# Kernel optimization log

Measured on AMD Instinct MI355X. Metric: run time of the kernel, lower is better.

The kernel has to match this reference:

```python
import jax, jax.numpy as jnp
import numpy as np

N, E, D = 50000, 800000, 128
H, C = 8, 16  # heads, hidden_per_head; H*C == D
NEG_SLOPE = 0.15


def setup_inputs() -> dict:
    key = jax.random.key(0)
    ks = jax.random.split(key, 8)
    x = jax.random.normal(ks[0], (N, D), dtype=jnp.float32)
    edge_index = jax.random.randint(ks[1], (2, E), 0, N, dtype=jnp.int32)
    s = 1.0 / np.sqrt(D)
    return {
        "x": x,
        "edge_index": edge_index,
        "ln_g": jnp.ones((D,), jnp.float32),
        "ln_b": jnp.zeros((D,), jnp.float32),
        "W_l": jax.random.normal(ks[2], (D, H * C), jnp.float32) * s,
        "b_l": jnp.zeros((H * C,), jnp.float32),
        "W_r": jax.random.normal(ks[3], (D, H * C), jnp.float32) * s,
        "b_r": jnp.zeros((H * C,), jnp.float32),
        "att": jax.random.normal(ks[4], (H, C), jnp.float32) * (1.0 / np.sqrt(C)),
        "bias": jnp.zeros((H * C,), jnp.float32),
    }


def _layernorm(x, g, b, eps=1e-5):
    mu = jnp.mean(x, axis=-1, keepdims=True)
    var = jnp.mean(jnp.square(x - mu), axis=-1, keepdims=True)
    return (x - mu) * jax.lax.rsqrt(var + eps) * g + b


def reference(x, edge_index, ln_g, ln_b, W_l, b_l, W_r, b_r, att, bias):
    src, dst = edge_index[0], edge_index[1]
    h = _layernorm(x, ln_g, ln_b)                      # [N, D]
    xl = (h @ W_l + b_l).reshape(N, H, C)              # source-side transform
    xr = (h @ W_r + b_r).reshape(N, H, C)              # target-side transform
    # GATv2 edge attention: leaky_relu(x_j + x_i) . att
    e = xl[src] + xr[dst]                              # [E, H, C]
    e_act = jnp.where(e > 0, e, NEG_SLOPE * e)
    alpha = jnp.einsum('ehc,hc->eh', e_act, att)       # [E, H]
    # segment softmax over edges grouped by destination node
    m = jax.ops.segment_max(alpha, dst, num_segments=N)   # [N, H]
    ex = jnp.exp(alpha - m[dst])                           # [E, H]
    denom = jax.ops.segment_sum(ex, dst, num_segments=N)  # [N, H]
    a = ex / (denom[dst] + 1e-16)                          # [E, H]
    # weighted message aggregation (scatter-add)
    msg = xl[src] * a[:, :, None]                          # [E, H, C]
    out = jax.ops.segment_sum(msg, dst, num_segments=N)   # [N, H, C]
    out = out.reshape(N, H * C) + bias
    h2 = jax.nn.relu(out)                                  # act='relu', dropout off (eval)
    return x + h2                                          # proj is Identity (in_dim == out_dim)
```

## Files before the change

### kernel.cpp

```cpp
#include <hip/hip_runtime.h>

typedef unsigned int uint32;
typedef __attribute__((ext_vector_type(4))) float f32x4;
typedef __attribute__((ext_vector_type(8))) short bf16x8;

#define NEG_SLOPE 0.15f
#define GPB 2

__device__ __forceinline__ float2 bf2_to_f2(uint32 u) {
  union { uint32 i; float f; } a, b;
  a.i = u << 16;
  b.i = u & 0xffff0000u;
  return make_float2(a.f, b.f);
}

__device__ __forceinline__ float bf_to_f(unsigned short s) {
  union { uint32 i; float f; } u;
  u.i = ((uint32)s) << 16;
  return u.f;
}

__device__ __forceinline__ unsigned short f32_to_bf16(float f) {
  union { float f; uint32 i; } u; u.f = f;
  uint32 r = u.i + 0x7fffu + ((u.i >> 16) & 1u);
  return (unsigned short)(r >> 16);
}

__device__ __forceinline__ uint32 pack_bf2(float x, float y) {
  return (uint32)f32_to_bf16(x) | ((uint32)f32_to_bf16(y) << 16);
}

__device__ __forceinline__ float2 loadpair(const void* p, size_t i, int isbf) {
  if (isbf) return bf2_to_f2(((const uint32*)p)[i]);
  return ((const float2*)p)[i];
}

__device__ __forceinline__ float loadelem(const void* p, size_t i, int isbf) {
  if (isbf) return bf_to_f(((const unsigned short*)p)[i]);
  return ((const float*)p)[i];
}

__device__ __forceinline__ int get_isbf(const void* ln_g) {
  return ((const uint32*)ln_g)[0] != 0x3F800000u ? 1 : 0;
}

__global__ __launch_bounds__(256) void prep_k(
    const void* __restrict__ Wl, const void* __restrict__ Wr,
    const void* __restrict__ att, const void* __restrict__ obias,
    const void* __restrict__ ln_g,
    unsigned short* __restrict__ Wt, float* __restrict__ att_c,
    float* __restrict__ obias_c)
{
  int isbf = get_isbf(ln_g);
  int id = blockIdx.x * 256 + threadIdx.x;
  int n = id >> 7, k = id & 127;
  float g = loadelem(ln_g, k, isbf);
  float v = (n < 128) ? loadelem(Wl, (size_t)k * 128 + n, isbf)
                      : loadelem(Wr, (size_t)k * 128 + (n - 128), isbf);
  Wt[(size_t)n * 128 + k] = f32_to_bf16(g * v);
  if (id < 128) {
    att_c[id]   = loadelem(att, id, isbf);
    obias_c[id] = loadelem(obias, id, isbf);
  }
}

__global__ __launch_bounds__(64) void prep2_k(
    const void* __restrict__ Wl, const void* __restrict__ Wr,
    const void* __restrict__ bl, const void* __restrict__ br,
    const void* __restrict__ ln_g, const void* __restrict__ ln_b,
    float* __restrict__ c1, float* __restrict__ c2b)
{
  int isbf = get_isbf(ln_g);
  int n = blockIdx.x;
  int lane = threadIdx.x;
  const void* W = (n < 128) ? Wl : Wr;
  int nn = n & 127;
  float s1 = 0.f, s2 = 0.f;
  #pragma unroll
  for (int t = 0; t < 2; ++t) {
    int kk = t * 64 + lane;
    float wv = loadelem(W, (size_t)kk * 128 + nn, isbf);
    s1 += loadelem(ln_g, kk, isbf) * wv;
    s2 += loadelem(ln_b, kk, isbf) * wv;
  }
  #pragma unroll
  for (int off = 1; off < 64; off <<= 1) {
    s1 += __shfl_xor(s1, off, 64);
    s2 += __shfl_xor(s2, off, 64);
  }
  if (lane == 0) {
    c1[n] = s1;
    c2b[n] = s2 + ((n < 128) ? loadelem(bl, nn, isbf) : loadelem(br, nn, isbf));
  }
}

__device__ __forceinline__ void load_group(bf16x8* slot, const void* x,
                                           int isbf, int rl, int quad) {
  if (isbf) {
    const unsigned short* xp = (const unsigned short*)x + (size_t)rl * 128 + quad * 8;
    #pragma unroll
    for (int kc = 0; kc < 4; ++kc) slot[kc] = *(const bf16x8*)(xp + kc * 32);
  } else {
    const float* xp = (const float*)x + (size_t)rl * 128 + quad * 8;
    #pragma unroll
    for (int kc = 0; kc < 4; ++kc) {
      float4 a0 = *(const float4*)(xp + kc * 32);
      float4 a1 = *(const float4*)(xp + kc * 32 + 4);
      union { bf16x8 v; uint32 u[4]; } av;
      av.u[0] = pack_bf2(a0.x, a0.y);
      av.u[1] = pack_bf2(a0.z, a0.w);
      av.u[2] = pack_bf2(a1.x, a1.y);
      av.u[3] = pack_bf2(a1.z, a1.w);
      slot[kc] = av.v;
    }
  }
}

__global__ __launch_bounds__(256) void ln_gemm_k(
    const void* __restrict__ x, const void* __restrict__ ln_g,
    const unsigned short* __restrict__ Wt,
    const float* __restrict__ c1, const float* __restrict__ c2b,
    unsigned short* __restrict__ xl,
    unsigned short* __restrict__ xr,
    int nrows)
{
  int isbf = get_isbf(ln_g);
  int lane = threadIdx.x & 63;
  int w    = threadIdx.x >> 6;
  int m16  = lane & 15;
  int quad = lane >> 4;
  int base = blockIdx.x * (GPB * 16);

  bf16x8 araw[GPB][4];
  #pragma unroll
  for (int g2 = 0; g2 < GPB; ++g2) {
    int r = base + g2 * 16 + m16;
    if (r >= nrows) r = nrows - 1;
    load_group(araw[g2], x, isbf, r, quad);
  }

  bf16x8 bfrag[4][4];
  #pragma unroll
  for (int nt = 0; nt < 4; ++nt)
    #pragma unroll
    for (int kc = 0; kc < 4; ++kc)
      bfrag[nt][kc] = *(const bf16x8*)(
          Wt + (size_t)(w * 64 + nt * 16 + m16) * 128 + kc * 32 + quad * 8);

  float c1v[4], c2v[4];
  #pragma unroll
  for (int nt = 0; nt < 4; ++nt) {
    int col = w * 64 + nt * 16 + m16;
    c1v[nt] = c1[col];
    c2v[nt] = c2b[col];
  }

  unsigned short* dst = (w < 2) ? xl : xr;
  int cb = (w & 1) * 64;

  #pragma unroll
  for (int g2 = 0; g2 < GPB; ++g2) {
    bf16x8* A = araw[g2];

    float s = 0.f, s2 = 0.f;
    #pragma unroll
    for (int kc = 0; kc < 4; ++kc) {
      union { bf16x8 v; uint32 u[4]; } uu; uu.v = A[kc];
      #pragma unroll
      for (int j = 0; j < 4; ++j) {
        float2 t = bf2_to_f2(uu.u[j]);
        s += t.x + t.y;
        s2 += t.x * t.x + t.y * t.y;
      }
    }
    s  += __shfl_xor(s, 16, 64);  s2 += __shfl_xor(s2, 16, 64);
    s  += __shfl_xor(s, 32, 64);  s2 += __shfl_xor(s2, 32, 64);
    float mu  = s * (1.0f / 128.0f);
    float var = fmaxf(s2 * (1.0f / 128.0f) - mu * mu, 0.0f);
    float rs  = rsqrtf(var + 1e-5f);
    float rm  = rs * mu;

    f32x4 acc[4];
    #pragma unroll
    for (int nt = 0; nt < 4; ++nt) acc[nt] = (f32x4){0.f, 0.f, 0.f, 0.f};
    #pragma unroll
    for (int kc = 0; kc < 4; ++kc)
      #pragma unroll
      for (int nt = 0; nt < 4; ++nt)
        acc[nt] = __builtin_amdgcn_mfma_f32_16x16x32_bf16(A[kc], bfrag[nt][kc], acc[nt], 0, 0, 0);

    float rs_j[4], rm_j[4];
    #pragma unroll
    for (int j = 0; j < 4; ++j) {
      rs_j[j] = __shfl(rs, quad * 4 + j, 64);
      rm_j[j] = __shfl(rm, quad * 4 + j, 64);
    }

    #pragma unroll
    for (int nt = 0; nt < 4; ++nt) {
      #pragma unroll
      for (int j = 0; j < 4; ++j) {
        int r = base + g2 * 16 + quad * 4 + j;
        if (r < nrows)
          dst[(size_t)r * 128 + cb + nt * 16 + m16] =
              f32_to_bf16(rs_j[j] * acc[nt][j] - rm_j[j] * c1v[nt] + c2v[nt]);
      }
    }
  }
}

__global__ __launch_bounds__(256) void hist_k(
    const int* __restrict__ ei, int* __restrict__ cntg,
    int E, int Eb, int R)
{
  __shared__ int hist[256];
  int b = blockIdx.x, tid = threadIdx.x;
  hist[tid] = 0;
  __syncthreads();
  int start = b * Eb, end = min(E, start + Eb);
  for (int e = start + tid; e < end; e += 256)
    atomicAdd(&hist[((uint32)ei[E + e]) >> 8], 1);
  __syncthreads();
  if (tid < R) cntg[tid * 256 + b] = hist[tid];
}

__global__ __launch_bounds__(1024) void scanA_k(const int* __restrict__ in,
    int* __restrict__ outl, int* __restrict__ psum, int n)
{
  __shared__ int wsum[16];
  int tid = threadIdx.x, lane = tid & 63, w = tid >> 6;
  int i = blockIdx.x * 1024 + tid;
  int v = (i < n) ? in[i] : 0;
  int xs = v;
  #pragma unroll
  for (int off = 1; off < 64; off <<= 1) {
    int y = __shfl_up(xs, off, 64);
    if (lane >= off) xs += y;
  }
  if (lane == 63) wsum[w] = xs;
  __syncthreads();
  if (w == 0) {
    int sv = (lane < 16) ? wsum[lane] : 0;
    int ss = sv;
    #pragma unroll
    for (int off = 1; off < 16; off <<= 1) {
      int y = __shfl_up(ss, off, 64);
      if (lane >= off) ss += y;
    }
    if (lane < 16) wsum[lane] = ss - sv;
    if (lane == 15) psum[blockIdx.x] = ss;
  }
  __syncthreads();
  if (i < n) outl[i] = wsum[w] + xs - v;
}

__global__ void scanB_k(int* __restrict__ psum, int* __restrict__ total, int nb) {
  int lane = threadIdx.x;
  int v = (lane < nb) ? psum[lane] : 0;
  int xs = v;
  #pragma unroll
  for (int off = 1; off < 64; off <<= 1) {
    int y = __shfl_up(xs, off, 64);
    if (lane >= off) xs += y;
  }
  if (lane < nb) psum[lane] = xs - v;
  if (lane == 63) *total = xs;
}

__global__ void scanC2_k(int* __restrict__ arr, const int* __restrict__ psum, int n) {
  int i = blockIdx.x * blockDim.x + threadIdx.x;
  if (i < n) arr[i] += psum[i >> 10];
}

__global__ __launch_bounds__(256) void binscatter_k(
    const int* __restrict__ ei, const int* __restrict__ cbase,
    uint32* __restrict__ binned, int E, int Eb, int R)
{
  __shared__ int cur[256];
  int b = blockIdx.x, tid = threadIdx.x;
  if (tid < R) cur[tid] = cbase[tid * 256 + b];
  __syncthreads();
  int start = b * Eb, end = min(E, start + Eb);
  for (int e = start + tid; e < end; e += 256) {
    uint32 src = (uint32)ei[e];
    uint32 dst = (uint32)ei[E + e];
    int pos = atomicAdd(&cur[dst >> 8], 1);
    binned[pos] = src | ((dst & 255u) << 16);
  }
}

__global__ __launch_bounds__(256) void rangesort_k(
    const uint32* __restrict__ binned, const int* __restrict__ cbase,
    int* __restrict__ starts, unsigned short* __restrict__ csr16,
    int E, int N, int R)
{
  __shared__ int hist[256];
  __shared__ int wsum[4];
  __shared__ int cur[256];
  int r = blockIdx.x;
  int tid = threadIdx.x, lane = tid & 63, w = tid >> 6;
  int segStart = cbase[r * 256];
  int segEnd = (r + 1 < R) ? cbase[(r + 1) * 256] : E;

  hist[tid] = 0;
  __syncthreads();
  for (int i = segStart + tid; i < segEnd; i += 256)
    atomicAdd(&hist[(binned[i] >> 16) & 255u], 1);
  __syncthreads();

  int v = hist[tid];
  int xs = v;
  #pragma unroll
  for (int off = 1; off < 64; off <<= 1) {
    int y = __shfl_up(xs, off, 64);
    if (lane >= off) xs += y;
  }
  if (lane == 63) wsum[w] = xs;
  __syncthreads();
  int woff = 0;
  #pragma unroll
  for (int i = 0; i < 4; ++i) if (i < w) woff += wsum[i];
  int st = segStart + woff + xs - v;
  int node = (r << 8) + tid;
  if (node < N) starts[node] = st;
  cur[tid] = st;
  __syncthreads();

  for (int i = segStart + tid; i < segEnd; i += 256) {
    uint32 pk = binned[i];
    int d = (pk >> 16) & 255u;
    int pos = atomicAdd(&cur[d], 1);
    csr16[pos] = (unsigned short)(pk & 0xffffu);
  }
}

__global__ __launch_bounds__(256) void agg_k(
    const uint32* __restrict__ xl32,
    const uint32* __restrict__ xr32,
    const int* __restrict__ starts, const unsigned short* __restrict__ csr16,
    const void* __restrict__ x, const void* __restrict__ ln_g,
    const float* __restrict__ att_c, const float* __restrict__ obias_c,
    void* __restrict__ out, int n)
{
  int node = blockIdx.x * 4 + (threadIdx.x >> 6);
  if (node >= n) return;
  int isbf = get_isbf(ln_g);
  int lane = threadIdx.x & 63;
  int q    = lane >> 4;
  int sub  = lane & 15;

  uint4 xru = *(const uint4*)(xr32 + (size_t)node * 64 + sub * 4);
  float2 r0 = bf2_to_f2(xru.x), r1 = bf2_to_f2(xru.y),
         r2 = bf2_to_f2(xru.z), r3 = bf2_to_f2(xru.w);
  float4 at0 = *(const float4*)(att_c + sub * 8);
  float4 at1 = *(const float4*)(att_c + sub * 8 + 4);

  float lsum = 0.f;
  float acc[8] = {0.f, 0.f, 0.f, 0.f, 0.f, 0.f, 0.f, 0.f};

  int p0 = starts[node], p1 = starts[node + 1];
  if (p0 < p1) {
    int pmax = p1 - 1;
    int pe = p0 + q;
    int idx = min(pe, pmax);
    bool valid = pe < p1;
    uint4 xu = *(const uint4*)(xl32 + (size_t)csr16[idx] * 64 + sub * 4);

    for (int p = p0; p < p1; p += 4) {
      int pen = p + 4 + q;
      int idxn = min(pen, pmax);
      uint4 xun = *(const uint4*)(xl32 + (size_t)csr16[idxn] * 64 + sub * 4);

      float2 a0 = bf2_to_f2(xu.x), a1 = bf2_to_f2(xu.y),
             a2 = bf2_to_f2(xu.z), a3 = bf2_to_f2(xu.w);
      float e0 = a0.x + r0.x, e1 = a0.y + r0.y, e2 = a1.x + r1.x, e3 = a1.y + r1.y;
      float e4 = a2.x + r2.x, e5 = a2.y + r2.y, e6 = a3.x + r3.x, e7 = a3.y + r3.y;
      e0 = fmaxf(e0, NEG_SLOPE * e0); e1 = fmaxf(e1, NEG_SLOPE * e1);
      e2 = fmaxf(e2, NEG_SLOPE * e2); e3 = fmaxf(e3, NEG_SLOPE * e3);
      e4 = fmaxf(e4, NEG_SLOPE * e4); e5 = fmaxf(e5, NEG_SLOPE * e5);
      e6 = fmaxf(e6, NEG_SLOPE * e6); e7 = fmaxf(e7, NEG_SLOPE * e7);
      float dot = e0 * at0.x + e1 * at0.y + e2 * at0.z + e3 * at0.w
                + e4 * at1.x + e5 * at1.y + e6 * at1.z + e7 * at1.w;
      dot += __shfl_xor(dot, 1, 64);
      float pw = valid ? __expf(dot) : 0.f;
      lsum += pw;
      acc[0] += pw * a0.x; acc[1] += pw * a0.y;
      acc[2] += pw * a1.x; acc[3] += pw * a1.y;
      acc[4] += pw * a2.x; acc[5] += pw * a2.y;
      acc[6] += pw * a3.x; acc[7] += pw * a3.y;

      xu = xun;
      valid = pen < p1;
    }
  }

  lsum += __shfl_xor(lsum, 16, 64);
  lsum += __shfl_xor(lsum, 32, 64);
  #pragma unroll
  for (int i = 0; i < 8; ++i) {
    acc[i] += __shfl_xor(acc[i], 16, 64);
    acc[i] += __shfl_xor(acc[i], 32, 64);
  }

  if (q == 0) {
    float inv = 1.0f / (lsum + 1e-16f);
    float4 b0 = *(const float4*)(obias_c + sub * 8);
    float4 b1 = *(const float4*)(obias_c + sub * 8 + 4);
    float2 rx[4];
    #pragma unroll
    for (int i = 0; i < 4; ++i)
      rx[i] = loadpair(x, (size_t)node * 64 + sub * 4 + i, isbf);
    float o0 = rx[0].x + fmaxf(acc[0] * inv + b0.x, 0.f);
    float o1 = rx[0].y + fmaxf(acc[1] * inv + b0.y, 0.f);
    float o2 = rx[1].x + fmaxf(acc[2] * inv + b0.z, 0.f);
    float o3 = rx[1].y + fmaxf(acc[3] * inv + b0.w, 0.f);
    float o4 = rx[2].x + fmaxf(acc[4] * inv + b1.x, 0.f);
    float o5 = rx[2].y + fmaxf(acc[5] * inv + b1.y, 0.f);
    float o6 = rx[3].x + fmaxf(acc[6] * inv + b1.z, 0.f);
    float o7 = rx[3].y + fmaxf(acc[7] * inv + b1.w, 0.f);
    if (isbf) {
      uint4 ov;
      ov.x = pack_bf2(o0, o1); ov.y = pack_bf2(o2, o3);
      ov.z = pack_bf2(o4, o5); ov.w = pack_bf2(o6, o7);
      *(uint4*)((uint32*)out + (size_t)node * 64 + sub * 4) = ov;
    } else {
      float4 f0 = make_float4(o0, o1, o2, o3);
      float4 f1 = make_float4(o4, o5, o6, o7);
      *(float4*)((float*)out + (size_t)node * 128 + sub * 8) = f0;
      *(float4*)((float*)out + (size_t)node * 128 + sub * 8 + 4) = f1;
    }
  }
}

static inline char* align16(char* p) {
  return (char*)(((uintptr_t)p + 15) & ~(uintptr_t)15);
}

extern "C" void kernel_launch(void* const* d_in, const int* in_sizes, int n_in,
                              void* d_out, int out_size, void* d_ws, size_t ws_size,
                              hipStream_t stream) {
  const void* x    = d_in[0];
  const int*  ei   = (const int*)d_in[1];
  const void* ln_g = d_in[2];
  const void* ln_b = d_in[3];
  const void* Wl   = d_in[4];
  const void* bl   = d_in[5];
  const void* Wr   = d_in[6];
  const void* br   = d_in[7];
  const void* att  = d_in[8];
  const void* bias = d_in[9];

  int N = in_sizes[0] / 128;
  int E = in_sizes[1] / 2;
  int R = (N + 255) >> 8;
  int L = R * 256;
  int Eb = (E + 255) / 256;

  char* ws = (char*)d_ws;
  unsigned short* xl = (unsigned short*)ws; ws = align16(ws + (size_t)N * 128 * 2);
  unsigned short* xr = (unsigned short*)ws; ws = align16(ws + (size_t)N * 128 * 2);
  unsigned short* Wt = (unsigned short*)ws; ws = align16(ws + 256 * 128 * 2);
  float* c1      = (float*)ws;              ws = align16(ws + 256 * 4);
  float* c2b     = (float*)ws;              ws = align16(ws + 256 * 4);
  float* att_c   = (float*)ws;              ws = align16(ws + 128 * 4);
  float* obias_c = (float*)ws;              ws = align16(ws + 128 * 4);
  int* cntg      = (int*)ws;                ws = align16(ws + (size_t)L * 4);
  int* cbase     = (int*)ws;                ws = align16(ws + (size_t)L * 4);
  int* psum      = (int*)ws;                ws = align16(ws + 64 * 4);
  int* starts    = (int*)ws;                ws = align16(ws + (size_t)(N + 1) * 4);
  uint32* binned = (uint32*)ws;             ws = align16(ws + (size_t)E * 4);
  unsigned short* csr16 = (unsigned short*)ws; ws = align16(ws + (size_t)E * 2);

  int nbScan = (L + 1023) / 1024;

  hipLaunchKernelGGL(prep_k, dim3(128), dim3(256), 0, stream,
                     Wl, Wr, att, bias, ln_g, Wt, att_c, obias_c);
  hipLaunchKernelGGL(prep2_k, dim3(256), dim3(64), 0, stream,
                     Wl, Wr, bl, br, ln_g, ln_b, c1, c2b);
  hipLaunchKernelGGL(hist_k, dim3(256), dim3(256), 0, stream, ei, cntg, E, Eb, R);
  hipLaunchKernelGGL(scanA_k, dim3(nbScan), dim3(1024), 0, stream, cntg, cbase, psum, L);
  hipLaunchKernelGGL(scanB_k, dim3(1), dim3(64), 0, stream, psum, starts + N, nbScan);
  hipLaunchKernelGGL(scanC2_k, dim3((L + 255) / 256), dim3(256), 0, stream, cbase, psum, L);
  hipLaunchKernelGGL(binscatter_k, dim3(256), dim3(256), 0, stream,
                     ei, cbase, binned, E, Eb, R);
  hipLaunchKernelGGL(rangesort_k, dim3(R), dim3(256), 0, stream,
                     binned, cbase, starts, csr16, E, N, R);
  hipLaunchKernelGGL(ln_gemm_k, dim3((N + GPB * 16 - 1) / (GPB * 16)), dim3(256), 0, stream,
                     x, ln_g, Wt, c1, c2b, xl, xr, N);
  hipLaunchKernelGGL(agg_k, dim3((N + 3) / 4), dim3(256), 0, stream,
                     (const uint32*)xl, (const uint32*)xr, starts, csr16,
                     x, ln_g, att_c, obias_c, d_out, N);
}
```

Measured before the change: 200.1 us.

## Merge prep kernels, vectorize edge loads, pack agg math, shrink GEMM groups

```diff
diff --git a/kernel.cpp b/kernel.cpp
--- a/kernel.cpp
+++ b/kernel.cpp
@@ -2,10 +2,11 @@
 
 typedef unsigned int uint32;
 typedef __attribute__((ext_vector_type(4))) float f32x4;
+typedef __attribute__((ext_vector_type(2))) float f32x2;
 typedef __attribute__((ext_vector_type(8))) short bf16x8;
 
 #define NEG_SLOPE 0.15f
-#define GPB 2
+#define GPB 1
 
 __device__ __forceinline__ float2 bf2_to_f2(uint32 u) {
   union { uint32 i; float f; } a, b;
@@ -14,6 +15,16 @@
   return make_float2(a.f, b.f);
 }
 
+__device__ __forceinline__ f32x2 unpk(uint32 u) {
+  union { uint32 i; float f; } lo, hi;
+  lo.i = u << 16; hi.i = u & 0xffff0000u;
+  f32x2 r; r.x = lo.f; r.y = hi.f; return r;
+}
+
+__device__ __forceinline__ f32x2 vmax2(f32x2 a, f32x2 b) {
+  f32x2 r; r.x = fmaxf(a.x, b.x); r.y = fmaxf(a.y, b.y); return r;
+}
+
 __device__ __forceinline__ float bf_to_f(unsigned short s) {
   union { uint32 i; float f; } u;
   u.i = ((uint32)s) << 16;
@@ -44,53 +55,50 @@
   return ((const uint32*)ln_g)[0] != 0x3F800000u ? 1 : 0;
 }
 
-__global__ __launch_bounds__(256) void prep_k(
-    const void* __restrict__ Wl, const void* __restrict__ Wr,
-    const void* __restrict__ att, const void* __restrict__ obias,
-    const void* __restrict__ ln_g,
-    unsigned short* __restrict__ Wt, float* __restrict__ att_c,
-    float* __restrict__ obias_c)
-{
-  int isbf = get_isbf(ln_g);
-  int id = blockIdx.x * 256 + threadIdx.x;
-  int n = id >> 7, k = id & 127;
-  float g = loadelem(ln_g, k, isbf);
-  float v = (n < 128) ? loadelem(Wl, (size_t)k * 128 + n, isbf)
-                      : loadelem(Wr, (size_t)k * 128 + (n - 128), isbf);
-  Wt[(size_t)n * 128 + k] = f32_to_bf16(g * v);
-  if (id < 128) {
-    att_c[id]   = loadelem(att, id, isbf);
-    obias_c[id] = loadelem(obias, id, isbf);
-  }
-}
-
-__global__ __launch_bounds__(64) void prep2_k(
+__global__ __launch_bounds__(256) void prepAll_k(
     const void* __restrict__ Wl, const void* __restrict__ Wr,
     const void* __restrict__ bl, const void* __restrict__ br,
+    const void* __restrict__ att, const void* __restrict__ obias,
     const void* __restrict__ ln_g, const void* __restrict__ ln_b,
-    float* __restrict__ c1, float* __restrict__ c2b)
+    unsigned short* __restrict__ Wt, float* __restrict__ c1,
+    float* __restrict__ c2b, float* __restrict__ att_c,
+    float* __restrict__ obias_c)
 {
   int isbf = get_isbf(ln_g);
-  int n = blockIdx.x;
-  int lane = threadIdx.x;
-  const void* W = (n < 128) ? Wl : Wr;
-  int nn = n & 127;
-  float s1 = 0.f, s2 = 0.f;
-  #pragma unroll
-  for (int t = 0; t < 2; ++t) {
-    int kk = t * 64 + lane;
-    float wv = loadelem(W, (size_t)kk * 128 + nn, isbf);
-    s1 += loadelem(ln_g, kk, isbf) * wv;
-    s2 += loadelem(ln_b, kk, isbf) * wv;
-  }
-  #pragma unroll
-  for (int off = 1; off < 64; off <<= 1) {
-    s1 += __shfl_xor(s1, off, 64);
-    s2 += __shfl_xor(s2, off, 64);
-  }
-  if (lane == 0) {
-    c1[n] = s1;
-    c2b[n] = s2 + ((n < 128) ? loadelem(bl, nn, isbf) : loadelem(br, nn, isbf));
+  int b = blockIdx.x;
+  if (b < 128) {
+    int id = b * 256 + threadIdx.x;
+    int n = id >> 7, k = id & 127;
+    float g = loadelem(ln_g, k, isbf);
+    float v = (n < 128) ? loadelem(Wl, (size_t)k * 128 + n, isbf)
+                        : loadelem(Wr, (size_t)k * 128 + (n - 128), isbf);
+    Wt[(size_t)n * 128 + k] = f32_to_bf16(g * v);
+    if (id < 128) {
+      att_c[id]   = loadelem(att, id, isbf);
+      obias_c[id] = loadelem(obias, id, isbf);
+    }
+  } else {
+    int w = threadIdx.x >> 6, lane = threadIdx.x & 63;
+    int n = (b - 128) * 4 + w;
+    const void* W = (n < 128) ? Wl : Wr;
+    int nn = n & 127;
+    float s1 = 0.f, s2 = 0.f;
+    #pragma unroll
+    for (int t = 0; t < 2; ++t) {
+      int kk = t * 64 + lane;
+      float wv = loadelem(W, (size_t)kk * 128 + nn, isbf);
+      s1 += loadelem(ln_g, kk, isbf) * wv;
+      s2 += loadelem(ln_b, kk, isbf) * wv;
+    }
+    #pragma unroll
+    for (int off = 1; off < 64; off <<= 1) {
+      s1 += __shfl_xor(s1, off, 64);
+      s2 += __shfl_xor(s2, off, 64);
+    }
+    if (lane == 0) {
+      c1[n] = s1;
+      c2b[n] = s2 + ((n < 128) ? loadelem(bl, nn, isbf) : loadelem(br, nn, isbf));
+    }
   }
 }
 
@@ -217,9 +225,23 @@
   int b = blockIdx.x, tid = threadIdx.x;
   hist[tid] = 0;
   __syncthreads();
-  int start = b * Eb, end = min(E, start + Eb);
-  for (int e = start + tid; e < end; e += 256)
-    atomicAdd(&hist[((uint32)ei[E + e]) >> 8], 1);
+  int startE = b * Eb, endE = min(E, startE + Eb);
+  const int* dp = ei + E;
+  if (((E | startE) & 3) == 0) {
+    int nfull = (endE - startE) >> 2;
+    for (int g = tid; g < nfull; g += 256) {
+      int4 d = *(const int4*)(dp + startE + g * 4);
+      atomicAdd(&hist[((uint32)d.x) >> 8], 1);
+      atomicAdd(&hist[((uint32)d.y) >> 8], 1);
+      atomicAdd(&hist[((uint32)d.z) >> 8], 1);
+      atomicAdd(&hist[((uint32)d.w) >> 8], 1);
+    }
+    int rem0 = startE + nfull * 4;
+    if (rem0 + tid < endE) atomicAdd(&hist[((uint32)dp[rem0 + tid]) >> 8], 1);
+  } else {
+    for (int e = startE + tid; e < endE; e += 256)
+      atomicAdd(&hist[((uint32)dp[e]) >> 8], 1);
+  }
   __syncthreads();
   if (tid < R) cntg[tid * 256 + b] = hist[tid];
 }
@@ -280,12 +302,35 @@
   int b = blockIdx.x, tid = threadIdx.x;
   if (tid < R) cur[tid] = cbase[tid * 256 + b];
   __syncthreads();
-  int start = b * Eb, end = min(E, start + Eb);
-  for (int e = start + tid; e < end; e += 256) {
-    uint32 src = (uint32)ei[e];
-    uint32 dst = (uint32)ei[E + e];
-    int pos = atomicAdd(&cur[dst >> 8], 1);
-    binned[pos] = src | ((dst & 255u) << 16);
+  int startE = b * Eb, endE = min(E, startE + Eb);
+  if (((E | startE) & 3) == 0) {
+    int nfull = (endE - startE) >> 2;
+    for (int g = tid; g < nfull; g += 256) {
+      int e = startE + g * 4;
+      int4 s = *(const int4*)(ei + e);
+      int4 d = *(const int4*)(ei + E + e);
+      int p0 = atomicAdd(&cur[((uint32)d.x) >> 8], 1);
+      binned[p0] = (uint32)s.x | (((uint32)d.x & 255u) << 16);
+      int p1 = atomicAdd(&cur[((uint32)d.y) >> 8], 1);
+      binned[p1] = (uint32)s.y | (((uint32)d.y & 255u) << 16);
+      int p2 = atomicAdd(&cur[((uint32)d.z) >> 8], 1);
+      binned[p2] = (uint32)s.z | (((uint32)d.z & 255u) << 16);
+      int p3 = atomicAdd(&cur[((uint32)d.w) >> 8], 1);
+      binned[p3] = (uint32)s.w | (((uint32)d.w & 255u) << 16);
+    }
+    int rem0 = startE + nfull * 4;
+    if (rem0 + tid < endE) {
+      int e = rem0 + tid;
+      uint32 src = (uint32)ei[e], dst = (uint32)ei[E + e];
+      int pos = atomicAdd(&cur[dst >> 8], 1);
+      binned[pos] = src | ((dst & 255u) << 16);
+    }
+  } else {
+    for (int e = startE + tid; e < endE; e += 256) {
+      uint32 src = (uint32)ei[e], dst = (uint32)ei[E + e];
+      int pos = atomicAdd(&cur[dst >> 8], 1);
+      binned[pos] = src | ((dst & 255u) << 16);
+    }
   }
 }
 
@@ -350,44 +395,46 @@
   int sub  = lane & 15;
 
   uint4 xru = *(const uint4*)(xr32 + (size_t)node * 64 + sub * 4);
-  float2 r0 = bf2_to_f2(xru.x), r1 = bf2_to_f2(xru.y),
-         r2 = bf2_to_f2(xru.z), r3 = bf2_to_f2(xru.w);
-  float4 at0 = *(const float4*)(att_c + sub * 8);
-  float4 at1 = *(const float4*)(att_c + sub * 8 + 4);
+  f32x2 xr0 = unpk(xru.x), xr1 = unpk(xru.y), xr2 = unpk(xru.z), xr3 = unpk(xru.w);
+  const f32x2* atp = (const f32x2*)(att_c + sub * 8);
+  f32x2 t0 = atp[0], t1 = atp[1], t2 = atp[2], t3 = atp[3];
+  f32x2 ns; ns.x = NEG_SLOPE; ns.y = NEG_SLOPE;
 
   float lsum = 0.f;
-  float acc[8] = {0.f, 0.f, 0.f, 0.f, 0.f, 0.f, 0.f, 0.f};
+  f32x2 ac[4];
+  #pragma unroll
+  for (int i = 0; i < 4; ++i) { ac[i].x = 0.f; ac[i].y = 0.f; }
 
   int p0 = starts[node], p1 = starts[node + 1];
   if (p0 < p1) {
     int pmax = p1 - 1;
     int pe = p0 + q;
-    int idx = min(pe, pmax);
     bool valid = pe < p1;
-    uint4 xu = *(const uint4*)(xl32 + (size_t)csr16[idx] * 64 + sub * 4);
+    uint4 xu = *(const uint4*)(xl32 + (size_t)csr16[min(pe, pmax)] * 64 + sub * 4);
 
     for (int p = p0; p < p1; p += 4) {
       int pen = p + 4 + q;
-      int idxn = min(pen, pmax);
-      uint4 xun = *(const uint4*)(xl32 + (size_t)csr16[idxn] * 64 + sub * 4);
-
-      float2 a0 = bf2_to_f2(xu.x), a1 = bf2_to_f2(xu.y),
-             a2 = bf2_to_f2(xu.z), a3 = bf2_to_f2(xu.w);
-      float e0 = a0.x + r0.x, e1 = a0.y + r0.y, e2 = a1.x + r1.x, e3 = a1.y + r1.y;
-      float e4 = a2.x + r2.x, e5 = a2.y + r2.y, e6 = a3.x + r3.x, e7 = a3.y + r3.y;
-      e0 = fmaxf(e0, NEG_SLOPE * e0); e1 = fmaxf(e1, NEG_SLOPE * e1);
-      e2 = fmaxf(e2, NEG_SLOPE * e2); e3 = fmaxf(e3, NEG_SLOPE * e3);
-      e4 = fmaxf(e4, NEG_SLOPE * e4); e5 = fmaxf(e5, NEG_SLOPE * e5);
-      e6 = fmaxf(e6, NEG_SLOPE * e6); e7 = fmaxf(e7, NEG_SLOPE * e7);
-      float dot = e0 * at0.x + e1 * at0.y + e2 * at0.z + e3 * at0.w
-                + e4 * at1.x + e5 * at1.y + e6 * at1.z + e7 * at1.w;
+      uint4 xun = *(const uint4*)(xl32 + (size_t)csr16[min(pen, pmax)] * 64 + sub * 4);
+
+      f32x2 a0 = unpk(xu.x), a1 = unpk(xu.y), a2 = unpk(xu.z), a3 = unpk(xu.w);
+      f32x2 e0 = a0 + xr0, e1 = a1 + xr1, e2 = a2 + xr2, e3 = a3 + xr3;
+      e0 = vmax2(e0, e0 * ns);
+      e1 = vmax2(e1, e1 * ns);
+      e2 = vmax2(e2, e2 * ns);
+      e3 = vmax2(e3, e3 * ns);
+      f32x2 dt = e0 * t0;
+      dt += e1 * t1;
+      dt += e2 * t2;
+      dt += e3 * t3;
+      float dot = dt.x + dt.y;
       dot += __shfl_xor(dot, 1, 64);
       float pw = valid ? __expf(dot) : 0.f;
       lsum += pw;
-      acc[0] += pw * a0.x; acc[1] += pw * a0.y;
-      acc[2] += pw * a1.x; acc[3] += pw * a1.y;
-      acc[4] += pw * a2.x; acc[5] += pw * a2.y;
-      acc[6] += pw * a3.x; acc[7] += pw * a3.y;
+      f32x2 pw2; pw2.x = pw; pw2.y = pw;
+      ac[0] += pw2 * a0;
+      ac[1] += pw2 * a1;
+      ac[2] += pw2 * a2;
+      ac[3] += pw2 * a3;
 
       xu = xun;
       valid = pen < p1;
@@ -397,9 +444,11 @@
   lsum += __shfl_xor(lsum, 16, 64);
   lsum += __shfl_xor(lsum, 32, 64);
   #pragma unroll
-  for (int i = 0; i < 8; ++i) {
-    acc[i] += __shfl_xor(acc[i], 16, 64);
-    acc[i] += __shfl_xor(acc[i], 32, 64);
+  for (int i = 0; i < 4; ++i) {
+    ac[i].x += __shfl_xor(ac[i].x, 16, 64);
+    ac[i].x += __shfl_xor(ac[i].x, 32, 64);
+    ac[i].y += __shfl_xor(ac[i].y, 16, 64);
+    ac[i].y += __shfl_xor(ac[i].y, 32, 64);
   }
 
   if (q == 0) {
@@ -410,14 +459,14 @@
     #pragma unroll
     for (int i = 0; i < 4; ++i)
       rx[i] = loadpair(x, (size_t)node * 64 + sub * 4 + i, isbf);
-    float o0 = rx[0].x + fmaxf(acc[0] * inv + b0.x, 0.f);
-    float o1 = rx[0].y + fmaxf(acc[1] * inv + b0.y, 0.f);
-    float o2 = rx[1].x + fmaxf(acc[2] * inv + b0.z, 0.f);
-    float o3 = rx[1].y + fmaxf(acc[3] * inv + b0.w, 0.f);
-    float o4 = rx[2].x + fmaxf(acc[4] * inv + b1.x, 0.f);
-    float o5 = rx[2].y + fmaxf(acc[5] * inv + b1.y, 0.f);
-    float o6 = rx[3].x + fmaxf(acc[6] * inv + b1.z, 0.f);
-    float o7 = rx[3].y + fmaxf(acc[7] * inv + b1.w, 0.f);
+    float o0 = rx[0].x + fmaxf(ac[0].x * inv + b0.x, 0.f);
+    float o1 = rx[0].y + fmaxf(ac[0].y * inv + b0.y, 0.f);
+    float o2 = rx[1].x + fmaxf(ac[1].x * inv + b0.z, 0.f);
+    float o3 = rx[1].y + fmaxf(ac[1].y * inv + b0.w, 0.f);
+    float o4 = rx[2].x + fmaxf(ac[2].x * inv + b1.x, 0.f);
+    float o5 = rx[2].y + fmaxf(ac[2].y * inv + b1.y, 0.f);
+    float o6 = rx[3].x + fmaxf(ac[3].x * inv + b1.z, 0.f);
+    float o7 = rx[3].y + fmaxf(ac[3].y * inv + b1.w, 0.f);
     if (isbf) {
       uint4 ov;
       ov.x = pack_bf2(o0, o1); ov.y = pack_bf2(o2, o3);
@@ -454,7 +503,7 @@
   int E = in_sizes[1] / 2;
   int R = (N + 255) >> 8;
   int L = R * 256;
-  int Eb = (E + 255) / 256;
+  int Eb = (((E + 255) / 256) + 3) & ~3;
 
   char* ws = (char*)d_ws;
   unsigned short* xl = (unsigned short*)ws; ws = align16(ws + (size_t)N * 128 * 2);
@@ -473,10 +522,9 @@
 
   int nbScan = (L + 1023) / 1024;
 
-  hipLaunchKernelGGL(prep_k, dim3(128), dim3(256), 0, stream,
-                     Wl, Wr, att, bias, ln_g, Wt, att_c, obias_c);
-  hipLaunchKernelGGL(prep2_k, dim3(256), dim3(64), 0, stream,
-                     Wl, Wr, bl, br, ln_g, ln_b, c1, c2b);
+  hipLaunchKernelGGL(prepAll_k, dim3(192), dim3(256), 0, stream,
+                     Wl, Wr, bl, br, att, bias, ln_g, ln_b,
+                     Wt, c1, c2b, att_c, obias_c);
   hipLaunchKernelGGL(hist_k, dim3(256), dim3(256), 0, stream, ei, cntg, E, Eb, R);
   hipLaunchKernelGGL(scanA_k, dim3(nbScan), dim3(1024), 0, stream, cntg, cbase, psum, L);
   hipLaunchKernelGGL(scanB_k, dim3(1), dim3(64), 0, stream, psum, starts + N, nbScan);
```

After: 202.2 us. Within noise of the previous version (+1.0%).
